# Performance work log

Measured on AMD Instinct MI355X. Metric: run time of the kernel, lower is better.

Reference implementation:

```python
import jax, jax.numpy as jnp
import numpy as np

SIZE = (128.0, 128.0, 128.0)
FEATURE_BLOCK_IDS = (1, 2, 3)


def _trilerp(feat, coords, power):
    # feat: [B, D, H, W, C]; coords: [B, N, 3] in [0, 1]
    B = coords.shape[0]
    scale = jnp.asarray([0.5 ** power * SIZE[0],
                         0.5 ** power * SIZE[1],
                         0.5 ** power * SIZE[2]], dtype=coords.dtype)
    hi = float(min(feat.shape[1:4])) - 1.01
    idx = jnp.clip(coords * scale, 0.01, hi)  # [B, N, 3]
    ix, iy, iz = idx[..., 0], idx[..., 1], idx[..., 2]
    x1, x2 = jnp.floor(ix), jnp.ceil(ix)
    y1, y2 = jnp.floor(iy), jnp.ceil(iy)
    z1, z2 = jnp.floor(iz), jnp.ceil(iz)
    b = jnp.arange(B)[:, None]  # broadcast batch index

    def g(xi, yi, zi):
        return feat[b, xi.astype(jnp.int32), yi.astype(jnp.int32), zi.astype(jnp.int32)]

    wx, wx2 = (ix - x1)[..., None], (x2 - ix)[..., None]
    wy, wy2 = (iy - y1)[..., None], (y2 - iy)[..., None]
    wz, wz2 = (iz - z1)[..., None], (z2 - iz)[..., None]

    # z = z1 plane
    lerp_x1 = g(x2, y1, z1) * wx + g(x1, y1, z1) * wx2
    lerp_x2 = g(x2, y2, z1) * wx + g(x1, y2, z1) * wx2
    lerp_y1 = lerp_x2 * wy + lerp_x1 * wy2
    # z = z2 plane
    lerp_x1 = g(x2, y1, z2) * wx + g(x1, y1, z2) * wx2
    lerp_x2 = g(x2, y2, z2) * wx + g(x1, y2, z2) * wx2
    lerp_y2 = lerp_x2 * wy + lerp_x1 * wy2
    return lerp_y2 * wz + lerp_y1 * wz2  # [B, N, C]


def setup_inputs() -> dict:
    key = jax.random.key(0)
    ks = jax.random.split(key, 7)
    B, N = 2, 50000
    return {
        'features0': jax.random.normal(ks[0], (B, 128, 128, 128, 1), jnp.float32),
        'features1': jax.random.normal(ks[1], (B, 64, 64, 64, 32), jnp.float32),
        'features2': jax.random.normal(ks[2], (B, 32, 32, 32, 64), jnp.float32),
        'features3': jax.random.normal(ks[3], (B, 16, 16, 16, 128), jnp.float32),
        'features4': jax.random.normal(ks[4], (B, 8, 8, 8, 256), jnp.float32),
        'mesh_coords': jax.random.uniform(ks[5], (B, N, 3), jnp.float32),
        'mesh_features': jax.random.normal(ks[6], (B, N, 3), jnp.float32),
    }


def reference(features0, features1, features2, features3, features4, mesh_coords, mesh_features):
    feats = [features0, features1, features2, features3, features4]
    # mesh_coords is [B, N, 3] -> one coord group, reshape is identity
    sampled = [_trilerp(feats[i], mesh_coords, i) for i in FEATURE_BLOCK_IDS]
    out = jnp.concatenate(sampled, axis=-1)
    return jnp.concatenate([out, mesh_features], axis=-1)
```

## Files before the change

### kernel.cpp

```cpp
#include <hip/hip_runtime.h>


__global__ __launch_bounds__(256) void trilerp_kernel(
    const float* __restrict__ f1,
    const float* __restrict__ f2,
    const float* __restrict__ f3,
    const float* __restrict__ coords,
    const float* __restrict__ meshf,
    float* __restrict__ out,
    int N)
{
    const int lane = threadIdx.x & 63;
    const int wv   = threadIdx.x >> 6;
    const int pn   = blockIdx.x * 4 + wv;
    if (pn >= N) return;
    const int b  = blockIdx.y;
    const int pt = b * N + pn;

    if (lane >= 56) {
        if (lane < 59) {
            __builtin_nontemporal_store(meshf[pt * 3 + (lane - 56)],
                                        &out[pt * 227 + 224 + (lane - 56)]);
        }
        return;
    }

    const float cx = coords[pt * 3 + 0];
    const float cy = coords[pt * 3 + 1];
    const float cz = coords[pt * 3 + 2];

    const float4* fp; int D, C4, c4, oc;
    if (lane < 8)       { fp = (const float4*)f1; D = 64; C4 = 8;  c4 = lane * 4;        oc = c4;      }
    else if (lane < 24) { fp = (const float4*)f2; D = 32; C4 = 16; c4 = (lane - 8) * 4;  oc = 32 + c4; }
    else                { fp = (const float4*)f3; D = 16; C4 = 32; c4 = (lane - 24) * 4; oc = 96 + c4; }

    const float scale = (float)D;
    const float hi    = (float)((double)D - 1.01);

    const float ix = fminf(fmaxf(cx * scale, 0.01f), hi);
    const float iy = fminf(fmaxf(cy * scale, 0.01f), hi);
    const float iz = fminf(fmaxf(cz * scale, 0.01f), hi);

    const float x1f = floorf(ix), x2f = ceilf(ix);
    const float y1f = floorf(iy), y2f = ceilf(iy);
    const float z1f = floorf(iz), z2f = ceilf(iz);
    const int x1 = (int)x1f, x2 = (int)x2f;
    const int y1 = (int)y1f, y2 = (int)y2f;
    const int z1 = (int)z1f, z2 = (int)z2f;

    const float wx = ix - x1f, wx2 = x2f - ix;
    const float wy = iy - y1f, wy2 = y2f - iy;
    const float wz = iz - z1f, wz2 = z2f - iz;

    const int base4 = b * (D * D * D * C4) + (c4 >> 2);
    #define IDX(X, Y, Z) (base4 + (((X) * D + (Y)) * D + (Z)) * C4)

    const float4 v111 = fp[IDX(x1, y1, z1)];
    const float4 v211 = fp[IDX(x2, y1, z1)];
    const float4 v121 = fp[IDX(x1, y2, z1)];
    const float4 v221 = fp[IDX(x2, y2, z1)];
    const float4 v112 = fp[IDX(x1, y1, z2)];
    const float4 v212 = fp[IDX(x2, y1, z2)];
    const float4 v122 = fp[IDX(x1, y2, z2)];
    const float4 v222 = fp[IDX(x2, y2, z2)];
    #undef IDX

    float4 r;
    {
        const float lx1a = v211.x * wx + v111.x * wx2;
        const float lx2a = v221.x * wx + v121.x * wx2;
        const float ly1  = lx2a * wy + lx1a * wy2;
        const float lx1b = v212.x * wx + v112.x * wx2;
        const float lx2b = v222.x * wx + v122.x * wx2;
        const float ly2  = lx2b * wy + lx1b * wy2;
        r.x = ly2 * wz + ly1 * wz2;
    }
    {
        const float lx1a = v211.y * wx + v111.y * wx2;
        const float lx2a = v221.y * wx + v121.y * wx2;
        const float ly1  = lx2a * wy + lx1a * wy2;
        const float lx1b = v212.y * wx + v112.y * wx2;
        const float lx2b = v222.y * wx + v122.y * wx2;
        const float ly2  = lx2b * wy + lx1b * wy2;
        r.y = ly2 * wz + ly1 * wz2;
    }
    {
        const float lx1a = v211.z * wx + v111.z * wx2;
        const float lx2a = v221.z * wx + v121.z * wx2;
        const float ly1  = lx2a * wy + lx1a * wy2;
        const float lx1b = v212.z * wx + v112.z * wx2;
        const float lx2b = v222.z * wx + v122.z * wx2;
        const float ly2  = lx2b * wy + lx1b * wy2;
        r.z = ly2 * wz + ly1 * wz2;
    }
    {
        const float lx1a = v211.w * wx + v111.w * wx2;
        const float lx2a = v221.w * wx + v121.w * wx2;
        const float ly1  = lx2a * wy + lx1a * wy2;
        const float lx1b = v212.w * wx + v112.w * wx2;
        const float lx2b = v222.w * wx + v122.w * wx2;
        const float ly2  = lx2b * wy + lx1b * wy2;
        r.w = ly2 * wz + ly1 * wz2;
    }

    float* o = out + pt * 227 + oc;
    __builtin_nontemporal_store(r.x, o + 0);
    __builtin_nontemporal_store(r.y, o + 1);
    __builtin_nontemporal_store(r.z, o + 2);
    __builtin_nontemporal_store(r.w, o + 3);
}

extern "C" void kernel_launch(void* const* d_in, const int* in_sizes, int n_in,
                              void* d_out, int out_size, void* d_ws, size_t ws_size,
                              hipStream_t stream) {
    const float* f1     = (const float*)d_in[1];
    const float* f2     = (const float*)d_in[2];
    const float* f3     = (const float*)d_in[3];
    const float* coords = (const float*)d_in[5];
    const float* meshf  = (const float*)d_in[6];
    float* out = (float*)d_out;

    const int B = in_sizes[1] / (64 * 64 * 64 * 32);
    const int N = in_sizes[5] / (B * 3);

    trilerp_kernel<<<dim3((N + 3) / 4, B), dim3(256), 0, stream>>>(
        f1, f2, f3, coords, meshf, out, N);
}
```

Baseline: 217.1 us.

## Split work by feature level into uniform blocks with a separate mesh-copy range

Instead of one wavefront per point with lanes divided across three levels (and 8 lanes idle), each block now handles a single level, with template-specialised D and channel count, and covers several points at full lane use. Mesh-feature copies move into their own trailing block range. The goal is to remove lane waste and per-lane branch divergence and to let the compiler fold constants. In exchange, coordinates are reloaded once per level, each level's outputs are written by different blocks (scattered partial writes into the same rows), and the batch index comes from a small per-thread loop.

```diff
diff --git a/kernel.cpp b/kernel.cpp
--- a/kernel.cpp
+++ b/kernel.cpp
@@ -1,38 +1,38 @@
 #include <hip/hip_runtime.h>
 
 
-__global__ __launch_bounds__(256) void trilerp_kernel(
-    const float* __restrict__ f1,
-    const float* __restrict__ f2,
-    const float* __restrict__ f3,
-    const float* __restrict__ coords,
-    const float* __restrict__ meshf,
-    float* __restrict__ out,
-    int N)
+__device__ __forceinline__ int point_batch(int p, int N) {
+    int b = 0;
+    while (p >= N) { p -= N; ++b; }
+    return b;
+}
+
+__device__ __forceinline__ float4 lerpw(const float4 a, const float4 b,
+                                        float w, float w2) {
+    float4 r;
+    r.x = a.x * w + b.x * w2;
+    r.y = a.y * w + b.y * w2;
+    r.z = a.z * w + b.z * w2;
+    r.w = a.w * w + b.w * w2;
+    return r;
+}
+
+template<int D, int LPP, int OCB>
+__device__ __forceinline__ void do_level(const float4* __restrict__ fp,
+                                         const float* __restrict__ coords,
+                                         float* __restrict__ out,
+                                         int pBase, int N, int P)
 {
-    const int lane = threadIdx.x & 63;
-    const int wv   = threadIdx.x >> 6;
-    const int pn   = blockIdx.x * 4 + wv;
-    if (pn >= N) return;
-    const int b  = blockIdx.y;
-    const int pt = b * N + pn;
+    const int tid  = threadIdx.x;
+    const int lane = tid & 63;
+    const int wv   = tid >> 6;
+    const int p    = pBase + wv * (64 / LPP) + (lane / LPP);
+    const int c4   = lane & (LPP - 1);
+    if (p >= P) return;
 
-    if (lane >= 56) {
-        if (lane < 59) {
-            __builtin_nontemporal_store(meshf[pt * 3 + (lane - 56)],
-                                        &out[pt * 227 + 224 + (lane - 56)]);
-        }
-        return;
-    }
-
-    const float cx = coords[pt * 3 + 0];
-    const float cy = coords[pt * 3 + 1];
-    const float cz = coords[pt * 3 + 2];
-
-    const float4* fp; int D, C4, c4, oc;
-    if (lane < 8)       { fp = (const float4*)f1; D = 64; C4 = 8;  c4 = lane * 4;        oc = c4;      }
-    else if (lane < 24) { fp = (const float4*)f2; D = 32; C4 = 16; c4 = (lane - 8) * 4;  oc = 32 + c4; }
-    else                { fp = (const float4*)f3; D = 16; C4 = 32; c4 = (lane - 24) * 4; oc = 96 + c4; }
+    const float cx = coords[p * 3 + 0];
+    const float cy = coords[p * 3 + 1];
+    const float cz = coords[p * 3 + 2];
 
     const float scale = (float)D;
     const float hi    = (float)((double)D - 1.01);
@@ -52,9 +52,8 @@
     const float wy = iy - y1f, wy2 = y2f - iy;
     const float wz = iz - z1f, wz2 = z2f - iz;
 
-    const int base4 = b * (D * D * D * C4) + (c4 >> 2);
-    #define IDX(X, Y, Z) (base4 + (((X) * D + (Y)) * D + (Z)) * C4)
-
+    const int base4 = point_batch(p, N) * (D * D * D * LPP) + c4;
+    #define IDX(X, Y, Z) (base4 + (((X) * D + (Y)) * D + (Z)) * LPP)
     const float4 v111 = fp[IDX(x1, y1, z1)];
     const float4 v211 = fp[IDX(x2, y1, z1)];
     const float4 v121 = fp[IDX(x1, y2, z1)];
@@ -65,49 +64,45 @@
     const float4 v222 = fp[IDX(x2, y2, z2)];
     #undef IDX
 
-    float4 r;
-    {
-        const float lx1a = v211.x * wx + v111.x * wx2;
-        const float lx2a = v221.x * wx + v121.x * wx2;
-        const float ly1  = lx2a * wy + lx1a * wy2;
-        const float lx1b = v212.x * wx + v112.x * wx2;
-        const float lx2b = v222.x * wx + v122.x * wx2;
-        const float ly2  = lx2b * wy + lx1b * wy2;
-        r.x = ly2 * wz + ly1 * wz2;
-    }
-    {
-        const float lx1a = v211.y * wx + v111.y * wx2;
-        const float lx2a = v221.y * wx + v121.y * wx2;
-        const float ly1  = lx2a * wy + lx1a * wy2;
-        const float lx1b = v212.y * wx + v112.y * wx2;
-        const float lx2b = v222.y * wx + v122.y * wx2;
-        const float ly2  = lx2b * wy + lx1b * wy2;
-        r.y = ly2 * wz + ly1 * wz2;
-    }
-    {
-        const float lx1a = v211.z * wx + v111.z * wx2;
-        const float lx2a = v221.z * wx + v121.z * wx2;
-        const float ly1  = lx2a * wy + lx1a * wy2;
-        const float lx1b = v212.z * wx + v112.z * wx2;
-        const float lx2b = v222.z * wx + v122.z * wx2;
-        const float ly2  = lx2b * wy + lx1b * wy2;
-        r.z = ly2 * wz + ly1 * wz2;
-    }
-    {
-        const float lx1a = v211.w * wx + v111.w * wx2;
-        const float lx2a = v221.w * wx + v121.w * wx2;
-        const float ly1  = lx2a * wy + lx1a * wy2;
-        const float lx1b = v212.w * wx + v112.w * wx2;
-        const float lx2b = v222.w * wx + v122.w * wx2;
-        const float ly2  = lx2b * wy + lx1b * wy2;
-        r.w = ly2 * wz + ly1 * wz2;
-    }
+    const float4 lx1a = lerpw(v211, v111, wx, wx2);
+    const float4 lx2a = lerpw(v221, v121, wx, wx2);
+    const float4 ly1  = lerpw(lx2a, lx1a, wy, wy2);
+    const float4 lx1b = lerpw(v212, v112, wx, wx2);
+    const float4 lx2b = lerpw(v222, v122, wx, wx2);
+    const float4 ly2  = lerpw(lx2b, lx1b, wy, wy2);
+    const float4 r    = lerpw(ly2,  ly1,  wz, wz2);
 
-    float* o = out + pt * 227 + oc;
+    float* o = out + p * 227 + OCB + c4 * 4;
     __builtin_nontemporal_store(r.x, o + 0);
     __builtin_nontemporal_store(r.y, o + 1);
     __builtin_nontemporal_store(r.z, o + 2);
     __builtin_nontemporal_store(r.w, o + 3);
+}
+
+__global__ __launch_bounds__(256) void trilerp_kernel(
+    const float* __restrict__ f1,
+    const float* __restrict__ f2,
+    const float* __restrict__ f3,
+    const float* __restrict__ coords,
+    const float* __restrict__ meshf,
+    float* __restrict__ out,
+    int N, int P, int nb1, int nb2, int nb3)
+{
+    const int blk = blockIdx.x;
+    if (blk < nb1) {
+        do_level<64, 8, 0>((const float4*)f1, coords, out, blk * 32, N, P);
+    } else if (blk < nb1 + nb2) {
+        do_level<32, 16, 32>((const float4*)f2, coords, out, (blk - nb1) * 16, N, P);
+    } else if (blk < nb1 + nb2 + nb3) {
+        do_level<16, 32, 96>((const float4*)f3, coords, out,
+                             (blk - nb1 - nb2) * 8, N, P);
+    } else {
+        const int e = (blk - nb1 - nb2 - nb3) * 256 + (int)threadIdx.x;
+        if (e < P * 3) {
+            const int p = e / 3, c = e - p * 3;
+            __builtin_nontemporal_store(meshf[e], &out[p * 227 + 224 + c]);
+        }
+    }
 }
 
 extern "C" void kernel_launch(void* const* d_in, const int* in_sizes, int n_in,
@@ -122,7 +117,14 @@
 
     const int B = in_sizes[1] / (64 * 64 * 64 * 32);
     const int N = in_sizes[5] / (B * 3);
+    const int P = B * N;
 
-    trilerp_kernel<<<dim3((N + 3) / 4, B), dim3(256), 0, stream>>>(
-        f1, f2, f3, coords, meshf, out, N);
+    const int nb1 = (P + 31) / 32;
+    const int nb2 = (P + 15) / 16;
+    const int nb3 = (P + 7) / 8;
+    const int nbm = (P * 3 + 255) / 256;
+    const int grid = nb1 + nb2 + nb3 + nbm;
+
+    trilerp_kernel<<<dim3(grid), dim3(256), 0, stream>>>(
+        f1, f2, f3, coords, meshf, out, N, P, nb1, nb2, nb3);
 }
```

After: 212.3 us. 1.02x faster.
